# Performance work log

Measured on AMD Instinct MI355X. Metric: run time of the kernel, lower is better.

## Reference

```python
import jax, jax.numpy as jnp
import numpy as np

EMBED_DIM = 1024
NUM_HEADS = 16
HEAD_DIM = EMBED_DIM // NUM_HEADS
B, T = 2, 2048


def setup_inputs() -> dict:
    key = jax.random.key(0)
    ks = jax.random.split(key, 9)
    s = 1.0 / np.sqrt(EMBED_DIM)
    x = jax.random.normal(ks[0], (B, T, EMBED_DIM), dtype=jnp.float32)
    Wq = jax.random.uniform(ks[1], (EMBED_DIM, EMBED_DIM), jnp.float32, -s, s)
    bq = jax.random.uniform(ks[2], (EMBED_DIM,), jnp.float32, -s, s)
    Wk = jax.random.uniform(ks[3], (EMBED_DIM, EMBED_DIM), jnp.float32, -s, s)
    bk = jax.random.uniform(ks[4], (EMBED_DIM,), jnp.float32, -s, s)
    Wv = jax.random.uniform(ks[5], (EMBED_DIM, EMBED_DIM), jnp.float32, -s, s)
    bv = jax.random.uniform(ks[6], (EMBED_DIM,), jnp.float32, -s, s)
    Wo = jax.random.uniform(ks[7], (EMBED_DIM, EMBED_DIM), jnp.float32, -s, s)
    bo = jax.random.uniform(ks[8], (EMBED_DIM,), jnp.float32, -s, s)
    return {"x": x, "Wq": Wq, "bq": bq, "Wk": Wk, "bk": bk,
            "Wv": Wv, "bv": bv, "Wo": Wo, "bo": bo}


def reference(x, Wq, bq, Wk, bk, Wv, bv, Wo, bo):
    Bx, Tx, D = x.shape
    # projections (torch Linear: y = x @ W^T + b); here W stored as [in, out]
    q = (x @ Wq + bq).reshape(Bx, Tx, NUM_HEADS, HEAD_DIM).transpose(0, 2, 1, 3)
    k = (x @ Wk + bk).reshape(Bx, Tx, NUM_HEADS, HEAD_DIM).transpose(0, 2, 1, 3)
    v = (x @ Wv + bv).reshape(Bx, Tx, NUM_HEADS, HEAD_DIM).transpose(0, 2, 1, 3)
    scale = HEAD_DIM ** -0.5
    attn = jnp.einsum('bhqd,bhkd->bhqk', q, k) * scale  # [B, H, T, T]
    causal = jnp.tril(jnp.ones((Tx, Tx), dtype=bool))
    attn = jnp.where(causal[None, None], attn, -jnp.inf)
    attn = jax.nn.softmax(attn, axis=-1)
    out = jnp.einsum('bhqk,bhkd->bhqd', attn, v)  # [B, H, T, hd]
    out = out.transpose(0, 2, 1, 3).reshape(Bx, Tx, D)
    return out @ Wo + bo
```

## Files before the change

### kernel.cpp

```cpp
#include <hip/hip_runtime.h>

#define EMBED 1024
#define NHEADS 16
#define HDIM 64
#define SEQ 2048
#define BATCH 2
#define MROWS (BATCH * SEQ)

using bf16x8 = __attribute__((ext_vector_type(8))) short;
using f32x4  = __attribute__((ext_vector_type(4))) float;
using us4    = __attribute__((ext_vector_type(4))) unsigned short;
using u32x2  = __attribute__((ext_vector_type(2))) unsigned int;

__device__ __forceinline__ unsigned short f2bf(float f) {
    unsigned int u = __builtin_bit_cast(unsigned int, f);
    u = (u + 0x7fffu + ((u >> 16) & 1u)) >> 16;
    return (unsigned short)u;
}

__device__ __forceinline__ unsigned int cvt_pk_bf16(float a, float b) {
    unsigned int d;
    asm("v_cvt_pk_bf16_f32 %0, %1, %2" : "=v"(d) : "v"(a), "v"(b));
    return d;
}

__device__ __forceinline__ void async16(const unsigned short* g, unsigned short* l) {
    __builtin_amdgcn_global_load_lds(
        (const __attribute__((address_space(1))) void*)g,
        (__attribute__((address_space(3))) void*)l, 16, 0, 0);
}

__global__ __launch_bounds__(256)
void cvt_x(const float* __restrict__ in, unsigned short* __restrict__ out)
{
    int i = blockIdx.x * 256 + threadIdx.x;
    float4 v = ((const float4*)in)[i];
    us4 o;
    o[0] = f2bf(v.x); o[1] = f2bf(v.y); o[2] = f2bf(v.z); o[3] = f2bf(v.w);
    ((us4*)out)[i] = o;
}

__global__ __launch_bounds__(256)
void cvt_w(const float* __restrict__ W0, const float* __restrict__ W1,
           const float* __restrict__ W2, const float* __restrict__ W3,
           unsigned short* __restrict__ T0, unsigned short* __restrict__ T1,
           unsigned short* __restrict__ T2, unsigned short* __restrict__ T3)
{
    const float* W = blockIdx.z == 0 ? W0 : blockIdx.z == 1 ? W1 :
                     blockIdx.z == 2 ? W2 : W3;
    unsigned short* T = blockIdx.z == 0 ? T0 : blockIdx.z == 1 ? T1 :
                        blockIdx.z == 2 ? T2 : T3;
    __shared__ unsigned short tile[64][72];
    const int tid = threadIdx.x;
    const int k0 = blockIdx.y << 6, n0 = blockIdx.x << 6;
    const int lr = tid >> 4, lc = (tid & 15) << 2;
#pragma unroll
    for (int it = 0; it < 4; ++it) {
        int kr = lr + it * 16;
        float4 v = *(const float4*)(W + (size_t)(k0 + kr) * EMBED + n0 + lc);
        tile[lc + 0][kr] = f2bf(v.x);
        tile[lc + 1][kr] = f2bf(v.y);
        tile[lc + 2][kr] = f2bf(v.z);
        tile[lc + 3][kr] = f2bf(v.w);
    }
    __syncthreads();
#pragma unroll
    for (int it = 0; it < 4; ++it) {
        int nr = lr + it * 16;
        us4 o = *(const us4*)(&tile[nr][lc]);
        *(us4*)(T + (size_t)(n0 + nr) * EMBED + k0 + lc) = o;
    }
}

__device__ __forceinline__ void mfma_gemm_core(
    const unsigned short* __restrict__ A, const unsigned short* __restrict__ Bt,
    int bm, int n0, unsigned short* As, unsigned short* Bs,
    int wv, int lane, f32x4 acc[4][4])
{
    const int m16 = lane & 15, quad = lane >> 4;
    const int mb = (wv >> 1) << 6;
    const int nb = (wv & 1) << 6;
    const int rsw = m16 & 7;

    const int gcol = ((lane & 7) ^ ((lane >> 3) & 7)) << 3;
    const unsigned short* ga = A  + (size_t)(bm + wv * 32 + (lane >> 3)) * EMBED + gcol;
    const unsigned short* gb = Bt + (size_t)(n0 + wv * 32 + (lane >> 3)) * EMBED + gcol;

    int offA[4], offB[4];
#pragma unroll
    for (int i = 0; i < 4; ++i) {
        offA[i] = (mb + i * 16 + m16) * 64;
        offB[i] = (nb + i * 16 + m16) * 64;
    }

    const int NK = EMBED / 64;
#define STAGE(t) do {                                                        \
        unsigned short* la = As + ((t) & 1) * (128 * 64) + wv * 32 * 64;     \
        unsigned short* lb = Bs + ((t) & 1) * (128 * 64) + wv * 32 * 64;     \
        const unsigned short* gat = ga + (t) * 64;                           \
        const unsigned short* gbt = gb + (t) * 64;                           \
        _Pragma("unroll")                                                    \
        for (int j = 0; j < 4; ++j) {                                        \
            async16(gat + j * 8 * EMBED, la + j * 8 * 64);                   \
            async16(gbt + j * 8 * EMBED, lb + j * 8 * 64);                   \
        }                                                                    \
    } while (0)

    STAGE(0);
    for (int t = 0; t < NK; ++t) {
        if (t + 1 < NK) {
            STAGE(t + 1);
            asm volatile("s_waitcnt vmcnt(8)" ::: "memory");
        } else {
            asm volatile("s_waitcnt vmcnt(0)" ::: "memory");
        }
        asm volatile("s_barrier" ::: "memory");
        const unsigned short* Ab = As + (t & 1) * (128 * 64);
        const unsigned short* Bb = Bs + (t & 1) * (128 * 64);
#pragma unroll
        for (int ks = 0; ks < 2; ++ks) {
            const int sl = (((ks << 2) + quad) ^ rsw) << 3;
            bf16x8 af[4], bfv[4];
#pragma unroll
            for (int i = 0; i < 4; ++i) {
                af[i]  = *(const bf16x8*)(Ab + offA[i] + sl);
                bfv[i] = *(const bf16x8*)(Bb + offB[i] + sl);
            }
#pragma unroll
            for (int i = 0; i < 4; ++i)
#pragma unroll
                for (int j = 0; j < 4; ++j)
                    acc[i][j] = __builtin_amdgcn_mfma_f32_16x16x32_bf16(
                        af[i], bfv[j], acc[i][j], 0, 0, 0);
        }
        asm volatile("s_barrier" ::: "memory");
    }
#undef STAGE
}

__device__ __forceinline__ void mfma_gemm_core64(
    const unsigned short* __restrict__ A, const unsigned short* __restrict__ Bt,
    int bm, int n0, unsigned short* As, unsigned short* Bs,
    int wv, int lane, f32x4 acc[4][2])
{
    const int m16 = lane & 15, quad = lane >> 4;
    const int mb = (wv >> 1) << 6;
    const int nb = (wv & 1) << 5;
    const int rsw = m16 & 7;

    const int gcol = ((lane & 7) ^ ((lane >> 3) & 7)) << 3;
    const unsigned short* ga = A  + (size_t)(bm + wv * 32 + (lane >> 3)) * EMBED + gcol;
    const unsigned short* gb = Bt + (size_t)(n0 + wv * 16 + (lane >> 3)) * EMBED + gcol;

    int offA[4], offB[2];
#pragma unroll
    for (int i = 0; i < 4; ++i) offA[i] = (mb + i * 16 + m16) * 64;
#pragma unroll
    for (int j = 0; j < 2; ++j) offB[j] = (nb + j * 16 + m16) * 64;

    const int NK = EMBED / 64;
#define STAGE64(t) do {                                                      \
        unsigned short* la = As + ((t) & 1) * (128 * 64) + wv * 32 * 64;     \
        unsigned short* lb = Bs + ((t) & 1) * (64 * 64) + wv * 16 * 64;      \
        const unsigned short* gat = ga + (t) * 64;                           \
        const unsigned short* gbt = gb + (t) * 64;                           \
        _Pragma("unroll")                                                    \
        for (int j = 0; j < 4; ++j)                                          \
            async16(gat + j * 8 * EMBED, la + j * 8 * 64);                   \
        _Pragma("unroll")                                                    \
        for (int j = 0; j < 2; ++j)                                          \
            async16(gbt + j * 8 * EMBED, lb + j * 8 * 64);                   \
    } while (0)

    STAGE64(0);
    for (int t = 0; t < NK; ++t) {
        if (t + 1 < NK) {
            STAGE64(t + 1);
            asm volatile("s_waitcnt vmcnt(6)" ::: "memory");
        } else {
            asm volatile("s_waitcnt vmcnt(0)" ::: "memory");
        }
        asm volatile("s_barrier" ::: "memory");
        const unsigned short* Ab = As + (t & 1) * (128 * 64);
        const unsigned short* Bb = Bs + (t & 1) * (64 * 64);
#pragma unroll
        for (int ks = 0; ks < 2; ++ks) {
            const int sl = (((ks << 2) + quad) ^ rsw) << 3;
            bf16x8 af[4], bfv[2];
#pragma unroll
            for (int i = 0; i < 4; ++i)
                af[i] = *(const bf16x8*)(Ab + offA[i] + sl);
#pragma unroll
            for (int j = 0; j < 2; ++j)
                bfv[j] = *(const bf16x8*)(Bb + offB[j] + sl);
#pragma unroll
            for (int i = 0; i < 4; ++i)
#pragma unroll
                for (int j = 0; j < 2; ++j)
                    acc[i][j] = __builtin_amdgcn_mfma_f32_16x16x32_bf16(
                        af[i], bfv[j], acc[i][j], 0, 0, 0);
        }
        asm volatile("s_barrier" ::: "memory");
    }
#undef STAGE64
}

__global__ __launch_bounds__(256)
void qkv_gemm(const unsigned short* __restrict__ xb,
              const unsigned short* __restrict__ Wtq,
              const unsigned short* __restrict__ Wtk,
              const unsigned short* __restrict__ Wtv,
              const float* __restrict__ bq, const float* __restrict__ bk,
              const float* __restrict__ bv,
              unsigned short* __restrict__ Qo, unsigned short* __restrict__ Ko,
              unsigned short* __restrict__ Vto)
{
    __shared__ __align__(16) unsigned short As[2 * 128 * 64];
    __shared__ __align__(16) unsigned short Bs[2 * 128 * 64];
    const int tid = threadIdx.x, wv = tid >> 6, lane = tid & 63;
    const int m16 = lane & 15, quad = lane >> 4;
    const int which = blockIdx.x >> 3;
    const int n0 = (blockIdx.x & 7) << 7;
    const int bm = blockIdx.y << 7;
    const unsigned short* Bt = which == 0 ? Wtq : which == 1 ? Wtk : Wtv;
    const float* bias = which == 0 ? bq : which == 1 ? bk : bv;

    f32x4 acc[4][4];
#pragma unroll
    for (int i = 0; i < 4; ++i)
#pragma unroll
        for (int j = 0; j < 4; ++j) acc[i][j] = (f32x4){0.f, 0.f, 0.f, 0.f};

    mfma_gemm_core(xb, Bt, bm, n0, As, Bs, wv, lane, acc);

    const int mb = (wv >> 1) << 6, nb = (wv & 1) << 6;
    const float qscale = 0.125f * 1.4426950408889634f;
#pragma unroll
    for (int i = 0; i < 4; ++i) {
        const int m0 = bm + mb + i * 16 + quad * 4;
        const int b = m0 >> 11, t0 = m0 & (SEQ - 1);
#pragma unroll
        for (int j = 0; j < 4; ++j) {
            const int n = n0 + nb + j * 16 + m16;
            const int h = n >> 6, d = n & 63;
            const float bval = bias[n];
            if (which == 2) {
                us4 v;
#pragma unroll
                for (int r = 0; r < 4; ++r) v[r] = f2bf(acc[i][j][r] + bval);
                *(us4*)(Vto + ((((size_t)(b * NHEADS + h)) << 6) + d) * SEQ + t0) = v;
            } else {
                const float sc = which == 0 ? qscale : 1.f;
                unsigned short* dst = (which == 0 ? Qo : Ko) +
                    ((((size_t)(b * NHEADS + h)) << 11) + t0) * 64 + d;
#pragma unroll
                for (int r = 0; r < 4; ++r)
                    dst[(size_t)r * 64] = f2bf((acc[i][j][r] + bval) * sc);
            }
        }
    }
}

__global__ __launch_bounds__(256)
void out_gemm(const unsigned short* __restrict__ aob,
              const unsigned short* __restrict__ Wto,
              const float* __restrict__ bo, float* __restrict__ out)
{
    __shared__ __align__(16) unsigned short As[2 * 128 * 64];
    __shared__ __align__(16) unsigned short Bs[2 * 64 * 64];
    const int tid = threadIdx.x, wv = tid >> 6, lane = tid & 63;
    const int m16 = lane & 15, quad = lane >> 4;
    const int n0 = blockIdx.x << 6;
    const int bm = blockIdx.y << 7;

    f32x4 acc[4][2];
#pragma unroll
    for (int i = 0; i < 4; ++i)
#pragma unroll
        for (int j = 0; j < 2; ++j) acc[i][j] = (f32x4){0.f, 0.f, 0.f, 0.f};

    mfma_gemm_core64(aob, Wto, bm, n0, As, Bs, wv, lane, acc);

    const int mb = (wv >> 1) << 6, nb = (wv & 1) << 5;
#pragma unroll
    for (int i = 0; i < 4; ++i) {
        const int m0 = bm + mb + i * 16 + quad * 4;
#pragma unroll
        for (int j = 0; j < 2; ++j) {
            const int n = n0 + nb + j * 16 + m16;
            const float bval = bo[n];
#pragma unroll
            for (int r = 0; r < 4; ++r)
                out[(size_t)(m0 + r) * EMBED + n] = acc[i][j][r] + bval;
        }
    }
}

__global__ __launch_bounds__(256)
void attn_mfma(const unsigned short* __restrict__ Qb,
               const unsigned short* __restrict__ Kb,
               const unsigned short* __restrict__ Vtb,
               unsigned short* __restrict__ Oout)
{
    __shared__ __align__(16) unsigned short Ks[2][64 * 64];
    __shared__ __align__(16) unsigned short Vt[2][64 * 64];
    __shared__ __align__(16) unsigned short Ps[4][16 * 64];

    const int tid  = threadIdx.x;
    const int wv   = tid >> 6;
    const int lane = tid & 63;
    const int m16  = lane & 15;
    const int quad = lane >> 4;
    const int bh   = blockIdx.x;
    const int b    = bh >> 4, h = bh & 15;

    const int yr = blockIdx.y & 7, yk = blockIdx.y >> 3;
    const int qt = yk == 0 ? yr : yk == 1 ? 15 - yr : yk == 2 ? 16 + yr : 31 - yr;
    const int q0 = qt << 6;

    const int srow = tid >> 2;
    const int cc   = tid & 3;
    const int swr  = srow & 7;
    const int sx   = m16 & 7;

    bf16x8 rk0, rk1, rv0, rv1;
    auto load_tile = [&](int k0) {
        const int scol = cc << 4;
        const unsigned short* sk = Kb + (((size_t)bh << 11) + k0 + srow) * 64 + scol;
        rk0 = *(const bf16x8*)sk;
        rk1 = *(const bf16x8*)(sk + 8);
        const unsigned short* sv = Vtb + (((size_t)bh << 6) + srow) * SEQ + k0 + scol;
        rv0 = *(const bf16x8*)sv;
        rv1 = *(const bf16x8*)(sv + 8);
    };

    const size_t qoff =
        (((size_t)bh << 11) + q0 + (wv << 4) + m16) * 64 + (quad << 3);
    bf16x8 qa0 = *(const bf16x8*)(Qb + qoff);
    bf16x8 qa1 = *(const bf16x8*)(Qb + qoff + 32);

    f32x4 o[4];
#pragma unroll
    for (int dt = 0; dt < 4; ++dt) o[dt] = (f32x4){0.f, 0.f, 0.f, 0.f};
    float m_ = -1e30f, l_ = 0.f;

    load_tile(0);

    for (int kt = 0; kt <= qt; ++kt) {
        unsigned short* Kp = Ks[kt & 1];
        unsigned short* Vp = Vt[kt & 1];
        {
            unsigned short* kd = Kp + srow * 64;
            unsigned short* vd = Vp + srow * 64;
            *(bf16x8*)(kd + (((2 * cc) ^ swr) << 3))     = rk0;
            *(bf16x8*)(kd + (((2 * cc + 1) ^ swr) << 3)) = rk1;
            *(bf16x8*)(vd + (((2 * cc) ^ swr) << 3))     = rv0;
            *(bf16x8*)(vd + (((2 * cc + 1) ^ swr) << 3)) = rv1;
        }
        __syncthreads();
        if (kt < qt) load_tile((kt + 1) << 6);

        const bool diag = (kt == qt);

        f32x4 s[4];
#pragma unroll
        for (int g = 0; g < 4; ++g) {
            if (diag && g > wv) {
                s[g] = (f32x4){-1e30f, -1e30f, -1e30f, -1e30f};
                continue;
            }
            const unsigned short* kr = Kp + (g * 16 + m16) * 64;
            bf16x8 kb0 = *(const bf16x8*)(kr + ((quad ^ sx) << 3));
            bf16x8 kb1 = *(const bf16x8*)(kr + (((quad + 4) ^ sx) << 3));
            s[g] = (f32x4){0.f, 0.f, 0.f, 0.f};
            s[g] = __builtin_amdgcn_mfma_f32_16x16x32_bf16(kb0, qa0, s[g], 0, 0, 0);
            s[g] = __builtin_amdgcn_mfma_f32_16x16x32_bf16(kb1, qa1, s[g], 0, 0, 0);
        }
        if (diag) {
#pragma unroll
            for (int r = 0; r < 4; ++r)
                if (quad * 4 + r > m16) s[wv][r] = -1e30f;
        }

        float mx = fmaxf(fmaxf(s[0][0], s[0][1]), fmaxf(s[0][2], s[0][3]));
#pragma unroll
        for (int g = 1; g < 4; ++g)
            mx = fmaxf(mx, fmaxf(fmaxf(s[g][0], s[g][1]), fmaxf(s[g][2], s[g][3])));
        mx = fmaxf(mx, __shfl_xor(mx, 16));
        mx = fmaxf(mx, __shfl_xor(mx, 32));

        if (mx > m_ + 8.f) {
            const float alpha = exp2f(m_ - mx);
            m_ = mx;
            l_ *= alpha;
#pragma unroll
            for (int dt = 0; dt < 4; ++dt) o[dt] *= alpha;
        }

        float sum = 0.f;
        unsigned int pw0[4], pw1[4];
#pragma unroll
        for (int g = 0; g < 4; ++g) {
            float p0 = exp2f(s[g][0] - m_);
            float p1 = exp2f(s[g][1] - m_);
            float p2 = exp2f(s[g][2] - m_);
            float p3 = exp2f(s[g][3] - m_);
            sum += (p0 + p1) + (p2 + p3);
            pw0[g] = cvt_pk_bf16(p0, p1);
            pw1[g] = cvt_pk_bf16(p2, p3);
        }
        sum += __shfl_xor(sum, 16);
        sum += __shfl_xor(sum, 32);
        l_ += sum;

        {
            unsigned short* pd = Ps[wv] + m16 * 64 + ((quad & 1) << 2);
#pragma unroll
            for (int g = 0; g < 4; ++g) {
                u32x2 w; w.x = pw0[g]; w.y = pw1[g];
                *(u32x2*)(pd + (((2 * g + (quad >> 1)) ^ sx) << 3)) = w;
            }
        }

        const unsigned short* pr = Ps[wv] + m16 * 64;
        bf16x8 pa0 = *(const bf16x8*)(pr + ((quad ^ sx) << 3));
        bf16x8 pa1 = *(const bf16x8*)(pr + (((quad + 4) ^ sx) << 3));
        const bool skip_hi = diag && (wv < 2);
#pragma unroll
        for (int dt = 0; dt < 4; ++dt) {
            const unsigned short* vr = Vp + (dt * 16 + m16) * 64;
            bf16x8 vb0 = *(const bf16x8*)(vr + ((quad ^ sx) << 3));
            o[dt] = __builtin_amdgcn_mfma_f32_16x16x32_bf16(vb0, pa0, o[dt], 0, 0, 0);
            if (!skip_hi) {
                bf16x8 vb1 = *(const bf16x8*)(vr + (((quad + 4) ^ sx) << 3));
                o[dt] = __builtin_amdgcn_mfma_f32_16x16x32_bf16(vb1, pa1, o[dt], 0, 0, 0);
            }
        }
    }

    const float inv = 1.f / l_;
    const int t = q0 + (wv << 4) + m16;
    unsigned short* dst =
        Oout + ((size_t)((b << 11) + t) << 10) + (h << 6) + (quad << 2);
#pragma unroll
    for (int dt = 0; dt < 4; ++dt) {
        u32x2 w;
        w.x = cvt_pk_bf16(o[dt][0] * inv, o[dt][1] * inv);
        w.y = cvt_pk_bf16(o[dt][2] * inv, o[dt][3] * inv);
        *(u32x2*)(dst + dt * 16) = w;
    }
}

extern "C" void kernel_launch(void* const* d_in, const int* in_sizes, int n_in,
                              void* d_out, int out_size, void* d_ws, size_t ws_size,
                              hipStream_t stream) {
    const float* x  = (const float*)d_in[0];
    const float* Wq = (const float*)d_in[1];
    const float* bq = (const float*)d_in[2];
    const float* Wk = (const float*)d_in[3];
    const float* bk = (const float*)d_in[4];
    const float* Wv = (const float*)d_in[5];
    const float* bv = (const float*)d_in[6];
    const float* Wo = (const float*)d_in[7];
    const float* bo = (const float*)d_in[8];
    float* out = (float*)d_out;

    const size_t HSZ = (size_t)MROWS * EMBED;
    const size_t WSZ = (size_t)EMBED * EMBED;
    unsigned short* qb  = (unsigned short*)d_ws;
    unsigned short* kb  = qb + HSZ;
    unsigned short* vtb = kb + HSZ;
    unsigned short* aob = vtb + HSZ;
    unsigned short* xb  = aob + HSZ;
    unsigned short* wtq = xb + HSZ;
    unsigned short* wtk = wtq + WSZ;
    unsigned short* wtv = wtk + WSZ;
    unsigned short* wto = wtv + WSZ;

    cvt_x<<<MROWS * EMBED / 1024, 256, 0, stream>>>(x, xb);
    cvt_w<<<dim3(16, 16, 4), 256, 0, stream>>>(Wq, Wk, Wv, Wo, wtq, wtk, wtv, wto);

    qkv_gemm<<<dim3(24, 32), 256, 0, stream>>>(xb, wtq, wtk, wtv, bq, bk, bv,
                                               qb, kb, vtb);

    attn_mfma<<<dim3(32, 32), 256, 0, stream>>>(qb, kb, vtb, aob);

    out_gemm<<<dim3(16, 32), 256, 0, stream>>>(aob, wto, bo, out);
}
```

Measured before the change: 202.8 us.

## Merge conversion kernels, halve GEMM K-tile, single-buffer attention K/V tiles

The x and weight bf16 conversion kernels are merged into one launch, with a fifth z-slice of the grid handling x. The 128x128 GEMM core now stages 32-wide K slices instead of 64, which halves LDS use and changes the swizzle, so more blocks may fit per CU at the cost of twice as many barriers per K loop. The attention kernel drops double-buffered K/V LDS tiles and adds a __syncthreads before each tile store, cutting LDS use but adding a block-wide barrier per iteration.

```diff
diff --git a/kernel.cpp b/kernel.cpp
--- a/kernel.cpp
+++ b/kernel.cpp
@@ -31,27 +31,30 @@
 }
 
 __global__ __launch_bounds__(256)
-void cvt_x(const float* __restrict__ in, unsigned short* __restrict__ out)
-{
-    int i = blockIdx.x * 256 + threadIdx.x;
-    float4 v = ((const float4*)in)[i];
-    us4 o;
-    o[0] = f2bf(v.x); o[1] = f2bf(v.y); o[2] = f2bf(v.z); o[3] = f2bf(v.w);
-    ((us4*)out)[i] = o;
-}
-
-__global__ __launch_bounds__(256)
-void cvt_w(const float* __restrict__ W0, const float* __restrict__ W1,
-           const float* __restrict__ W2, const float* __restrict__ W3,
-           unsigned short* __restrict__ T0, unsigned short* __restrict__ T1,
-           unsigned short* __restrict__ T2, unsigned short* __restrict__ T3)
-{
+void cvt_all(const float* __restrict__ X, unsigned short* __restrict__ XO,
+             const float* __restrict__ W0, const float* __restrict__ W1,
+             const float* __restrict__ W2, const float* __restrict__ W3,
+             unsigned short* __restrict__ T0, unsigned short* __restrict__ T1,
+             unsigned short* __restrict__ T2, unsigned short* __restrict__ T3)
+{
+    const int tid = threadIdx.x;
+    if (blockIdx.z == 4) {
+        const int blk = blockIdx.y * 16 + blockIdx.x;
+#pragma unroll
+        for (int it = 0; it < 16; ++it) {
+            int i = (blk * 16 + it) * 256 + tid;
+            float4 v = ((const float4*)X)[i];
+            us4 o;
+            o[0] = f2bf(v.x); o[1] = f2bf(v.y); o[2] = f2bf(v.z); o[3] = f2bf(v.w);
+            ((us4*)XO)[i] = o;
+        }
+        return;
+    }
     const float* W = blockIdx.z == 0 ? W0 : blockIdx.z == 1 ? W1 :
                      blockIdx.z == 2 ? W2 : W3;
     unsigned short* T = blockIdx.z == 0 ? T0 : blockIdx.z == 1 ? T1 :
                         blockIdx.z == 2 ? T2 : T3;
     __shared__ unsigned short tile[64][72];
-    const int tid = threadIdx.x;
     const int k0 = blockIdx.y << 6, n0 = blockIdx.x << 6;
     const int lr = tid >> 4, lc = (tid & 15) << 2;
 #pragma unroll
@@ -80,59 +83,56 @@
     const int m16 = lane & 15, quad = lane >> 4;
     const int mb = (wv >> 1) << 6;
     const int nb = (wv & 1) << 6;
-    const int rsw = m16 & 7;
-
-    const int gcol = ((lane & 7) ^ ((lane >> 3) & 7)) << 3;
-    const unsigned short* ga = A  + (size_t)(bm + wv * 32 + (lane >> 3)) * EMBED + gcol;
-    const unsigned short* gb = Bt + (size_t)(n0 + wv * 32 + (lane >> 3)) * EMBED + gcol;
+    const int rsw = m16 & 3;
+
+    const int srow0 = lane >> 2;
+    const int gcol  = ((lane & 3) ^ (srow0 & 3)) << 3;
+    const unsigned short* ga = A  + (size_t)(bm + wv * 16 + srow0) * EMBED + gcol;
+    const unsigned short* gb = Bt + (size_t)(n0 + wv * 16 + srow0) * EMBED + gcol;
 
     int offA[4], offB[4];
 #pragma unroll
     for (int i = 0; i < 4; ++i) {
-        offA[i] = (mb + i * 16 + m16) * 64;
-        offB[i] = (nb + i * 16 + m16) * 64;
-    }
-
-    const int NK = EMBED / 64;
+        offA[i] = (mb + i * 16 + m16) * 32;
+        offB[i] = (nb + i * 16 + m16) * 32;
+    }
+
+    const int NK = EMBED / 32;
 #define STAGE(t) do {                                                        \
-        unsigned short* la = As + ((t) & 1) * (128 * 64) + wv * 32 * 64;     \
-        unsigned short* lb = Bs + ((t) & 1) * (128 * 64) + wv * 32 * 64;     \
-        const unsigned short* gat = ga + (t) * 64;                           \
-        const unsigned short* gbt = gb + (t) * 64;                           \
-        _Pragma("unroll")                                                    \
-        for (int j = 0; j < 4; ++j) {                                        \
-            async16(gat + j * 8 * EMBED, la + j * 8 * 64);                   \
-            async16(gbt + j * 8 * EMBED, lb + j * 8 * 64);                   \
-        }                                                                    \
+        unsigned short* la = As + ((t) & 1) * (128 * 32) + wv * 16 * 32;     \
+        unsigned short* lb = Bs + ((t) & 1) * (128 * 32) + wv * 16 * 32;     \
+        const unsigned short* gat = ga + (t) * 32;                           \
+        const unsigned short* gbt = gb + (t) * 32;                           \
+        async16(gat, la);                                                    \
+        async16(gat + 64 * EMBED, la + 64 * 32);                             \
+        async16(gbt, lb);                                                    \
+        async16(gbt + 64 * EMBED, lb + 64 * 32);                             \
     } while (0)
 
     STAGE(0);
     for (int t = 0; t < NK; ++t) {
         if (t + 1 < NK) {
             STAGE(t + 1);
-            asm volatile("s_waitcnt vmcnt(8)" ::: "memory");
+            asm volatile("s_waitcnt vmcnt(4)" ::: "memory");
         } else {
             asm volatile("s_waitcnt vmcnt(0)" ::: "memory");
         }
         asm volatile("s_barrier" ::: "memory");
-        const unsigned short* Ab = As + (t & 1) * (128 * 64);
-        const unsigned short* Bb = Bs + (t & 1) * (128 * 64);
-#pragma unroll
-        for (int ks = 0; ks < 2; ++ks) {
-            const int sl = (((ks << 2) + quad) ^ rsw) << 3;
-            bf16x8 af[4], bfv[4];
-#pragma unroll
-            for (int i = 0; i < 4; ++i) {
-                af[i]  = *(const bf16x8*)(Ab + offA[i] + sl);
-                bfv[i] = *(const bf16x8*)(Bb + offB[i] + sl);
-            }
-#pragma unroll
-            for (int i = 0; i < 4; ++i)
-#pragma unroll
-                for (int j = 0; j < 4; ++j)
-                    acc[i][j] = __builtin_amdgcn_mfma_f32_16x16x32_bf16(
-                        af[i], bfv[j], acc[i][j], 0, 0, 0);
-        }
+        const unsigned short* Ab = As + (t & 1) * (128 * 32);
+        const unsigned short* Bb = Bs + (t & 1) * (128 * 32);
+        const int sl = ((quad ^ rsw) << 3);
+        bf16x8 af[4], bfv[4];
+#pragma unroll
+        for (int i = 0; i < 4; ++i) {
+            af[i]  = *(const bf16x8*)(Ab + offA[i] + sl);
+            bfv[i] = *(const bf16x8*)(Bb + offB[i] + sl);
+        }
+#pragma unroll
+        for (int i = 0; i < 4; ++i)
+#pragma unroll
+            for (int j = 0; j < 4; ++j)
+                acc[i][j] = __builtin_amdgcn_mfma_f32_16x16x32_bf16(
+                    af[i], bfv[j], acc[i][j], 0, 0, 0);
         asm volatile("s_barrier" ::: "memory");
     }
 #undef STAGE
@@ -215,8 +215,8 @@
               unsigned short* __restrict__ Qo, unsigned short* __restrict__ Ko,
               unsigned short* __restrict__ Vto)
 {
-    __shared__ __align__(16) unsigned short As[2 * 128 * 64];
-    __shared__ __align__(16) unsigned short Bs[2 * 128 * 64];
+    __shared__ __align__(16) unsigned short As[2 * 128 * 32];
+    __shared__ __align__(16) unsigned short Bs[2 * 128 * 32];
     const int tid = threadIdx.x, wv = tid >> 6, lane = tid & 63;
     const int m16 = lane & 15, quad = lane >> 4;
     const int which = blockIdx.x >> 3;
@@ -302,8 +302,8 @@
                const unsigned short* __restrict__ Vtb,
                unsigned short* __restrict__ Oout)
 {
-    __shared__ __align__(16) unsigned short Ks[2][64 * 64];
-    __shared__ __align__(16) unsigned short Vt[2][64 * 64];
+    __shared__ __align__(16) unsigned short Ks[64 * 64];
+    __shared__ __align__(16) unsigned short Vt[64 * 64];
     __shared__ __align__(16) unsigned short Ps[4][16 * 64];
 
     const int tid  = threadIdx.x;
@@ -347,11 +347,10 @@
     load_tile(0);
 
     for (int kt = 0; kt <= qt; ++kt) {
-        unsigned short* Kp = Ks[kt & 1];
-        unsigned short* Vp = Vt[kt & 1];
+        __syncthreads();
         {
-            unsigned short* kd = Kp + srow * 64;
-            unsigned short* vd = Vp + srow * 64;
+            unsigned short* kd = Ks + srow * 64;
+            unsigned short* vd = Vt + srow * 64;
             *(bf16x8*)(kd + (((2 * cc) ^ swr) << 3))     = rk0;
             *(bf16x8*)(kd + (((2 * cc + 1) ^ swr) << 3)) = rk1;
             *(bf16x8*)(vd + (((2 * cc) ^ swr) << 3))     = rv0;
@@ -369,7 +368,7 @@
                 s[g] = (f32x4){-1e30f, -1e30f, -1e30f, -1e30f};
                 continue;
             }
-            const unsigned short* kr = Kp + (g * 16 + m16) * 64;
+            const unsigned short* kr = Ks + (g * 16 + m16) * 64;
             bf16x8 kb0 = *(const bf16x8*)(kr + ((quad ^ sx) << 3));
             bf16x8 kb1 = *(const bf16x8*)(kr + (((quad + 4) ^ sx) << 3));
             s[g] = (f32x4){0.f, 0.f, 0.f, 0.f};
@@ -428,7 +427,7 @@
         const bool skip_hi = diag && (wv < 2);
 #pragma unroll
         for (int dt = 0; dt < 4; ++dt) {
-            const unsigned short* vr = Vp + (dt * 16 + m16) * 64;
+            const unsigned short* vr = Vt + (dt * 16 + m16) * 64;
             bf16x8 vb0 = *(const bf16x8*)(vr + ((quad ^ sx) << 3));
             o[dt] = __builtin_amdgcn_mfma_f32_16x16x32_bf16(vb0, pa0, o[dt], 0, 0, 0);
             if (!skip_hi) {
@@ -477,8 +476,8 @@
     unsigned short* wtv = wtk + WSZ;
     unsigned short* wto = wtv + WSZ;
 
-    cvt_x<<<MROWS * EMBED / 1024, 256, 0, stream>>>(x, xb);
-    cvt_w<<<dim3(16, 16, 4), 256, 0, stream>>>(Wq, Wk, Wv, Wo, wtq, wtk, wtv, wto);
+    cvt_all<<<dim3(16, 16, 5), 256, 0, stream>>>(x, xb, Wq, Wk, Wv, Wo,
+                                                 wtq, wtk, wtv, wto);
 
     qkv_gemm<<<dim3(24, 32), 256, 0, stream>>>(xb, wtq, wtk, wtv, bq, bk, bv,
                                                qb, kb, vtb);
```

Result: faster. 196.9 us (median of 2 runs) (-2.9%).
